# Kernel tuning notes

Measured on AMD Instinct MI355X. Metric: run time of the kernel, lower is better.

## Reference

```python
import jax, jax.numpy as jnp
import numpy as np

N = 50000       # nodes
E = 800000      # edges (before self loops)
F_IN = 256      # num_features
HID = 64        # hidden_dim
HEADS = 4       # num_heads
NEG = 0.2       # negative_slope
LN_EPS = 1e-5


def setup_inputs() -> dict:
    key = jax.random.key(0)
    ks = jax.random.split(key, 24)
    g = lambda k, shape, s=0.05: jax.random.normal(k, shape, jnp.float32) * s
    inp = {
        "x": jax.random.normal(ks[0], (N, F_IN), jnp.float32),
        "edge_index": jax.random.randint(ks[1], (2, E), 0, N, jnp.int32),
        # gat1: in=F_IN, out=HID per head, HEADS heads, concat=True
        "W1": g(ks[2], (HEADS * HID, F_IN)),
        "att_src1": g(ks[3], (HEADS, HID)),
        "att_dst1": g(ks[4], (HEADS, HID)),
        "b1": g(ks[5], (HEADS * HID,)),
        # gat2: in=HEADS*HID, out=HID, 1 head
        "W2": g(ks[6], (HID, HEADS * HID)),
        "att_src2": g(ks[7], (1, HID)),
        "att_dst2": g(ks[8], (1, HID)),
        "b2": g(ks[9], (HID,)),
        # lin_in residual projection
        "lin_w": g(ks[10], (HID, F_IN)),
        "lin_b": g(ks[11], (HID,)),
        # LayerNorm
        "gamma": jnp.ones((HID,), jnp.float32),
        "beta": jnp.zeros((HID,), jnp.float32),
        # GRU (1 layer, input=HID, hidden=HID), gate order r,z,n as in torch
        "w_ih": g(ks[12], (3 * HID, HID)),
        "w_hh": g(ks[13], (3 * HID, HID)),
        "b_ih": g(ks[14], (3 * HID,)),
        "b_hh": g(ks[15], (3 * HID,)),
        # fc head -> 3 classes
        "fc_w": g(ks[16], (3, HID)),
        "fc_b": g(ks[17], (3,)),
    }
    return inp


def gat_conv(x, W, att_src, att_dst, bias, src, dst, heads, n_nodes):
    """PyG-style GATConv (eval mode: no dropout). src/dst include self loops."""
    h = (x @ W.T).reshape(n_nodes, heads, -1)            # [N,H,C]
    a_src = jnp.einsum('nhc,hc->nh', h, att_src)          # [N,H]
    a_dst = jnp.einsum('nhc,hc->nh', h, att_dst)
    e = jax.nn.leaky_relu(a_src[src] + a_dst[dst], NEG)   # [E',H]
    m = jax.ops.segment_max(e, dst, num_segments=n_nodes) # scatter-softmax over dst
    e = jnp.exp(e - m[dst])
    s = jax.ops.segment_sum(e, dst, num_segments=n_nodes)
    alpha = e / s[dst]                                    # [E',H]
    out = jax.ops.segment_sum(alpha[:, :, None] * h[src], dst, num_segments=n_nodes)
    return out.reshape(n_nodes, -1) + bias                # concat heads + bias


def reference(x, edge_index, W1, att_src1, att_dst1, b1, W2, att_src2, att_dst2, b2,
              lin_w, lin_b, gamma, beta, w_ih, w_hh, b_ih, b_hh, fc_w, fc_b):
    n = x.shape[0]
    loops = jnp.arange(n, dtype=edge_index.dtype)
    src = jnp.concatenate([edge_index[0], loops])  # add_self_loops=True default
    dst = jnp.concatenate([edge_index[1], loops])

    h = jax.nn.leaky_relu(gat_conv(x, W1, att_src1, att_dst1, b1, src, dst, HEADS, n), NEG)
    # F.dropout is identity in eval mode
    h = gat_conv(h, W2, att_src2, att_dst2, b2, src, dst, 1, n)
    h = jax.nn.leaky_relu(h, NEG)
    # LayerNorm (torch uses biased variance)
    mu = h.mean(-1, keepdims=True)
    var = ((h - mu) ** 2).mean(-1, keepdims=True)
    h = (h - mu) / jnp.sqrt(var + LN_EPS) * gamma + beta
    h = h + x @ lin_w.T + lin_b
    # single-step GRU with h0 = 0 (seq_len == 1)
    gi = h @ w_ih.T + b_ih                 # [N,3C]
    i_r, i_z, i_n = jnp.split(gi, 3, axis=-1)
    h_r, h_z, h_n = jnp.split(b_hh, 3)     # W_hh @ 0 == 0
    r = jax.nn.sigmoid(i_r + h_r)
    z = jax.nn.sigmoid(i_z + h_z)
    ng = jnp.tanh(i_n + r * h_n)
    hy = (1.0 - z) * ng                    # + z * h_prev(=0)
    return hy @ fc_w.T + fc_b              # [N,3]
```

## Files before the change

kernel.cpp:

```cpp
#include <hip/hip_runtime.h>
#include <hip/hip_bf16.h>

#define N_NODES 50000
#define N_EDGES 800000
#define F_IN 256
#define HID 64
#define HEADS 4
#define NEG 0.2f
#define LN_EPS 1e-5f

typedef _Float16 half8 __attribute__((ext_vector_type(8)));
typedef _Float16 half4v __attribute__((ext_vector_type(4)));
typedef _Float16 half2v __attribute__((ext_vector_type(2)));
typedef float floatx4 __attribute__((ext_vector_type(4)));

union H2U { unsigned u; half2v h; };
union H8U { half8 v; half2v h2[4]; };

__device__ __forceinline__ float wave_sum(float v) {
    #pragma unroll
    for (int o = 32; o > 0; o >>= 1) v += __shfl_xor(v, o, 64);
    return v;
}
__device__ __forceinline__ float leaky(float x) { return x > 0.0f ? x : NEG * x; }

__global__ void prep_kernel(const int* __restrict__ src, const int* __restrict__ dst,
                            int* __restrict__ deg, int* __restrict__ colb,
                            const float* __restrict__ W1, const float* __restrict__ lin_w,
                            const float* __restrict__ W2, const float* __restrict__ w_ih,
                            _Float16* __restrict__ B1big, _Float16* __restrict__ W2h,
                            _Float16* __restrict__ w_ihh,
                            int E, int Etot, int SB) {
    if ((int)blockIdx.x < SB) {
        int e = blockIdx.x * 256 + threadIdx.x;
        if (e >= Etot) return;
        int s, d;
        if (e < E) { s = src[e]; d = dst[e]; }
        else       { s = d = e - E; }
        int pos = atomicAdd(&deg[d], 1);
        if (pos < 64) colb[d * 64 + pos] = s;
        return;
    }
    int rel = ((blockIdx.x - SB) * 256 + threadIdx.x) * 4;
    const float* s; _Float16* d;
    if      (rel < 65536) { s = W1; d = B1big; }
    else if ((rel -= 65536) < 16384) { s = lin_w; d = B1big + 65536; }
    else if ((rel -= 16384) < 16384) { s = W2; d = W2h; }
    else if ((rel -= 16384) < 12288) { s = w_ih; d = w_ihh; }
    else return;
    float4 v = *(const float4*)(s + rel);
    half4v h;
    h[0] = (_Float16)v.x; h[1] = (_Float16)v.y;
    h[2] = (_Float16)v.z; h[3] = (_Float16)v.w;
    *(half4v*)(d + rel) = h;
}

__device__ __forceinline__ half8 load_a8(const _Float16* p) { return *(const half8*)p; }
__device__ __forceinline__ half8 load_a8(const float* p) {
    float4 f0 = *(const float4*)p;
    float4 f1 = *(const float4*)(p + 4);
    half8 h;
    h[0] = (_Float16)f0.x; h[1] = (_Float16)f0.y;
    h[2] = (_Float16)f0.z; h[3] = (_Float16)f0.w;
    h[4] = (_Float16)f1.x; h[5] = (_Float16)f1.y;
    h[6] = (_Float16)f1.z; h[7] = (_Float16)f1.w;
    return h;
}

template<int NT, int H, typename OutT, typename AT>
__global__ __launch_bounds__(256, 2)
void gemm_mfma(const AT* __restrict__ A, const _Float16* __restrict__ B,
               const float* __restrict__ bias, OutT* __restrict__ Cout,
               const float* __restrict__ att_s, const float* __restrict__ att_d,
               float* __restrict__ a_srcO, float* __restrict__ a_dstO,
               int M, int K, int bias_mode) {
    constexpr int Nc = NT * 16;
    constexpr int BROW = 40;
    constexpr int BTILE = Nc * BROW * 2;
    constexpr int TILEB = 16 * Nc * sizeof(OutT);
    constexpr int SM = (BTILE > 4 * TILEB) ? BTILE : 4 * TILEB;
    __shared__ __align__(16) char smem[SM];
    _Float16* sB = (_Float16*)smem;
    int tid = threadIdx.x;
    int w = tid >> 6, lane = tid & 63;
    int m_base = blockIdx.x * 64 + w * 16;
    bool active = (m_base < M);
    int r = lane & 15, q = lane >> 4;
    const AT* ap = A + (size_t)(m_base + r) * K + q * 8;
    floatx4 acc[NT];
    #pragma unroll
    for (int t = 0; t < NT; ++t) acc[t] = (floatx4){0.f, 0.f, 0.f, 0.f};
    half8 a_next = {};
    if (active) a_next = load_a8(ap);
    for (int k0 = 0; k0 < K; k0 += 32) {
        for (int i = tid; i < Nc * 4; i += 256) {
            int row = i >> 2, seg = i & 3;
            *(half8*)(sB + row * BROW + seg * 8) =
                *(const half8*)(B + (size_t)row * K + k0 + seg * 8);
        }
        __syncthreads();
        half8 a = a_next;
        if (active && k0 + 32 < K) a_next = load_a8(ap + k0 + 32);
        if (active) {
            half8 b[NT];
            #pragma unroll
            for (int t = 0; t < NT; ++t)
                b[t] = *(const half8*)(sB + (t * 16 + r) * BROW + q * 8);
            #pragma unroll
            for (int t = 0; t < NT; ++t)
                acc[t] = __builtin_amdgcn_mfma_f32_16x16x32_f16(a, b[t], acc[t], 0, 0, 0);
        }
        __syncthreads();
    }
    if (active) {
        OutT* st = (OutT*)(smem + w * TILEB);
        #pragma unroll
        for (int t = 0; t < NT; ++t) {
            int cc = t * 16 + r;
            float bv = 0.f;
            if (bias_mode == 1) bv = bias[cc];
            else if (bias_mode == 2 && cc >= 256) bv = bias[cc - 256];
            #pragma unroll
            for (int rr = 0; rr < 4; ++rr)
                st[(q * 4 + rr) * Nc + cc] = (OutT)(acc[t][rr] + bv);
        }
        constexpr int NISS = TILEB / 1024;
        const int4* src = (const int4*)st;
        int4* dst = (int4*)((char*)Cout + (size_t)m_base * (Nc * sizeof(OutT)));
        #pragma unroll
        for (int i = 0; i < NISS; ++i) dst[i * 64 + lane] = src[i * 64 + lane];
        if constexpr (H > 0) {
            float ps[H][4], pd[H][4];
            #pragma unroll
            for (int h = 0; h < H; ++h) {
                #pragma unroll
                for (int rr = 0; rr < 4; ++rr) { ps[h][rr] = 0.f; pd[h][rr] = 0.f; }
                #pragma unroll
                for (int tt = 0; tt < 4; ++tt) {
                    int t = h * 4 + tt;
                    float as = att_s[t * 16 + r];
                    float ad = att_d[t * 16 + r];
                    #pragma unroll
                    for (int rr = 0; rr < 4; ++rr) {
                        ps[h][rr] += acc[t][rr] * as;
                        pd[h][rr] += acc[t][rr] * ad;
                    }
                }
            }
            #pragma unroll
            for (int m = 1; m < 16; m <<= 1) {
                #pragma unroll
                for (int h = 0; h < H; ++h)
                    #pragma unroll
                    for (int rr = 0; rr < 4; ++rr) {
                        ps[h][rr] += __shfl_xor(ps[h][rr], m, 64);
                        pd[h][rr] += __shfl_xor(pd[h][rr], m, 64);
                    }
            }
            if (r == 0) {
                #pragma unroll
                for (int rr = 0; rr < 4; ++rr) {
                    int gm = m_base + q * 4 + rr;
                    #pragma unroll
                    for (int h = 0; h < H; ++h) {
                        a_srcO[gm * H + h] = ps[h][rr];
                        a_dstO[gm * H + h] = pd[h][rr];
                    }
                }
            }
        }
    }
}

__global__ void gat_agg4(const _Float16* __restrict__ h, const float* __restrict__ a_src,
                         const float* __restrict__ a_dst, const int* __restrict__ degA,
                         const int* __restrict__ colb, const float* __restrict__ bias,
                         _Float16* __restrict__ outp, int N) {
    int w = threadIdx.x >> 6, lane = threadIdx.x & 63;
    int i = blockIdx.x * 4 + w;
    if (i >= N) return;
    __shared__ unsigned alphS[4][256];
    __shared__ int      scolS[4][64];
    unsigned* alph = alphS[w];
    int*      scol = scolS[w];
    int deg = degA[i];
    deg = deg > 64 ? 64 : deg;
    float4 ad4 = *(const float4*)(a_dst + i * 4);

    float e0 = 0.f, e1 = 0.f, e2 = 0.f, e3 = 0.f; int s = 0;
    if (lane < deg) {
        s = colb[i * 64 + lane];
        float4 as4 = *(const float4*)(a_src + (size_t)s * 4);
        e0 = __expf(leaky(as4.x + ad4.x));
        e1 = __expf(leaky(as4.y + ad4.y));
        e2 = __expf(leaky(as4.z + ad4.z));
        e3 = __expf(leaky(as4.w + ad4.w));
    }
    float s0 = wave_sum(e0), s1 = wave_sum(e1), s2 = wave_sum(e2), s3 = wave_sum(e3);
    float4 al = make_float4(0.f, 0.f, 0.f, 0.f);
    int so = 0;
    if (lane < deg) {
        al = make_float4(e0 / s0, e1 / s1, e2 / s2, e3 / s3);
        so = s * 640;
    }
    H2U p0, p1, p2, p3;
    _Float16 t0 = (_Float16)al.x; p0.h = (half2v){t0, t0};
    _Float16 t1 = (_Float16)al.y; p1.h = (half2v){t1, t1};
    _Float16 t2 = (_Float16)al.z; p2.h = (half2v){t2, t2};
    _Float16 t3 = (_Float16)al.w; p3.h = (half2v){t3, t3};
    *(uint4*)(alph + lane * 4) = make_uint4(p0.u, p1.u, p2.u, p3.u);
    scol[lane] = so;
    int half32 = lane >> 5;
    int fl = lane & 31;
    int flb = fl * 16;
    int ahofs = half32 * 4 + (fl >> 3);
    const char* hB = (const char*)h;
    float acc[8];
    #pragma unroll
    for (int k = 0; k < 8; ++k) acc[k] = 0.f;
    int dpad = (deg + 7) & ~7;
    for (int j = 0; j < dpad; j += 8) {
        int o0 = scol[j + half32];
        int o1 = scol[j + 2 + half32];
        int o2 = scol[j + 4 + half32];
        int o3 = scol[j + 6 + half32];
        H8U v0, v1, v2, v3;
        v0.v = *(const half8*)(hB + (flb + o0));
        v1.v = *(const half8*)(hB + (flb + o1));
        v2.v = *(const half8*)(hB + (flb + o2));
        v3.v = *(const half8*)(hB + (flb + o3));
        H2U a0, a1, a2, a3;
        a0.u = alph[j * 4 + ahofs];
        a1.u = alph[j * 4 + 8 + ahofs];
        a2.u = alph[j * 4 + 16 + ahofs];
        a3.u = alph[j * 4 + 24 + ahofs];
        #pragma unroll
        for (int p = 0; p < 4; ++p) {
            half2v hp = a0.h * v0.h2[p];
            hp = __builtin_elementwise_fma(a1.h, v1.h2[p], hp);
            hp = __builtin_elementwise_fma(a2.h, v2.h2[p], hp);
            hp = __builtin_elementwise_fma(a3.h, v3.h2[p], hp);
            acc[p * 2]     += (float)hp[0];
            acc[p * 2 + 1] += (float)hp[1];
        }
    }
    #pragma unroll
    for (int k = 0; k < 8; ++k) acc[k] += __shfl_xor(acc[k], 32, 64);
    if (lane < 32) {
        half8 o8;
        #pragma unroll
        for (int k = 0; k < 8; ++k)
            o8[k] = (_Float16)leaky(acc[k] + bias[fl * 8 + k]);
        *(half8*)(outp + (size_t)i * 256 + fl * 8) = o8;
    }
}

__global__ void gat_agg1_ln(const _Float16* __restrict__ h, const float* __restrict__ a_src,
                            const float* __restrict__ a_dst, const int* __restrict__ degA,
                            const int* __restrict__ colb, const float* __restrict__ bias,
                            const _Float16* __restrict__ linh, const float* __restrict__ gamma,
                            const float* __restrict__ beta, _Float16* __restrict__ hresh,
                            int N) {
    int w = threadIdx.x >> 6, lane = threadIdx.x & 63;
    int i = blockIdx.x * 4 + w;
    if (i >= N) return;
    __shared__ unsigned alphS[4][80];
    __shared__ int      scolS[4][80];
    unsigned* alph = alphS[w];
    int*      scol = scolS[w];
    int deg = degA[i];
    deg = deg > 64 ? 64 : deg;
    float ad = a_dst[i];
    int f0 = (lane & 7) * 8;
    float acc[8];
    #pragma unroll
    for (int k = 0; k < 8; ++k) acc[k] = 0.f;

    float e = 0.f; int s = 0;
    if (lane < deg) {
        s = colb[i * 64 + lane];
        e = __expf(leaky(a_src[s] + ad));
    }
    float ss = wave_sum(e);
    H2U pa; pa.u = 0;
    int so = 0;
    if (lane < deg) {
        _Float16 ah = (_Float16)(e / ss);
        pa.h = (half2v){ah, ah};
        so = s << 7;
    }
    alph[lane] = pa.u;
    scol[lane] = so;
    if (lane < 16) { alph[64 + lane] = 0; scol[64 + lane] = 0; }
    int g = lane >> 3;
    int fb = (lane & 7) * 16;
    const char* hB = (const char*)h;
    int dpad = (deg + 15) & ~15;
    for (int j = 0; j < dpad; j += 16) {
        int o0 = scol[j + g];
        int o1 = scol[j + 8 + g];
        H8U v0, v1;
        v0.v = *(const half8*)(hB + (fb + o0));
        v1.v = *(const half8*)(hB + (fb + o1));
        H2U a0, a1;
        a0.u = alph[j + g];
        a1.u = alph[j + 8 + g];
        #pragma unroll
        for (int p = 0; p < 4; ++p) {
            half2v hp = a0.h * v0.h2[p];
            hp = __builtin_elementwise_fma(a1.h, v1.h2[p], hp);
            acc[p * 2]     += (float)hp[0];
            acc[p * 2 + 1] += (float)hp[1];
        }
    }
    #pragma unroll
    for (int k = 0; k < 8; ++k) {
        acc[k] += __shfl_xor(acc[k], 8, 64);
        acc[k] += __shfl_xor(acc[k], 16, 64);
        acc[k] += __shfl_xor(acc[k], 32, 64);
    }
    float4 b0 = *(const float4*)(bias + f0);
    float4 b1 = *(const float4*)(bias + f0 + 4);
    float o[8];
    o[0] = leaky(acc[0] + b0.x); o[1] = leaky(acc[1] + b0.y);
    o[2] = leaky(acc[2] + b0.z); o[3] = leaky(acc[3] + b0.w);
    o[4] = leaky(acc[4] + b1.x); o[5] = leaky(acc[5] + b1.y);
    o[6] = leaky(acc[6] + b1.z); o[7] = leaky(acc[7] + b1.w);
    float ls = 0.f;
    #pragma unroll
    for (int k = 0; k < 8; ++k) ls += o[k];
    ls += __shfl_xor(ls, 1, 64); ls += __shfl_xor(ls, 2, 64); ls += __shfl_xor(ls, 4, 64);
    float mu = ls * (1.0f / 64.0f);
    float lq = 0.f;
    #pragma unroll
    for (int k = 0; k < 8; ++k) { o[k] -= mu; lq += o[k] * o[k]; }
    lq += __shfl_xor(lq, 1, 64); lq += __shfl_xor(lq, 2, 64); lq += __shfl_xor(lq, 4, 64);
    float rstd = rsqrtf(lq * (1.0f / 64.0f) + LN_EPS);
    float4 g0 = *(const float4*)(gamma + f0);
    float4 g1 = *(const float4*)(gamma + f0 + 4);
    float4 be0 = *(const float4*)(beta + f0);
    float4 be1 = *(const float4*)(beta + f0 + 4);
    half8 l8 = *(const half8*)(linh + (size_t)i * 320 + f0);
    if (lane < 8) {
        half8 hv;
        hv[0] = (_Float16)(o[0] * rstd * g0.x + be0.x + (float)l8[0]);
        hv[1] = (_Float16)(o[1] * rstd * g0.y + be0.y + (float)l8[1]);
        hv[2] = (_Float16)(o[2] * rstd * g0.z + be0.z + (float)l8[2]);
        hv[3] = (_Float16)(o[3] * rstd * g0.w + be0.w + (float)l8[3]);
        hv[4] = (_Float16)(o[4] * rstd * g1.x + be1.x + (float)l8[4]);
        hv[5] = (_Float16)(o[5] * rstd * g1.y + be1.y + (float)l8[5]);
        hv[6] = (_Float16)(o[6] * rstd * g1.z + be1.z + (float)l8[6]);
        hv[7] = (_Float16)(o[7] * rstd * g1.w + be1.w + (float)l8[7]);
        *(half8*)(hresh + (size_t)i * 64 + f0) = hv;
    }
}

__global__ __launch_bounds__(256, 2)
void gemm_gru(const _Float16* __restrict__ A, const _Float16* __restrict__ B,
              const float* __restrict__ b_ih, const float* __restrict__ b_hh,
              const float* __restrict__ fc_w, const float* __restrict__ fc_b,
              float* __restrict__ outp, int M) {
    const int K = 64, NT = 12, Nc = 192;
    constexpr int BROW = 40;
    __shared__ __align__(16) char smem[4 * 16 * 192 * 2];
    _Float16* sB = (_Float16*)smem;
    int tid = threadIdx.x;
    int w = tid >> 6, lane = tid & 63;
    int m_base = blockIdx.x * 64 + w * 16;
    bool active = (m_base < M);
    int r = lane & 15, q = lane >> 4;
    const _Float16* ap = A + (size_t)(m_base + r) * K + q * 8;
    floatx4 acc[NT];
    #pragma unroll
    for (int t = 0; t < NT; ++t) acc[t] = (floatx4){0.f, 0.f, 0.f, 0.f};
    half8 a_next = {};
    if (active) a_next = *(const half8*)ap;
    for (int k0 = 0; k0 < K; k0 += 32) {
        for (int i = tid; i < Nc * 4; i += 256) {
            int row = i >> 2, seg = i & 3;
            *(half8*)(sB + row * BROW + seg * 8) =
                *(const half8*)(B + (size_t)row * K + k0 + seg * 8);
        }
        __syncthreads();
        half8 a = a_next;
        if (active && k0 + 32 < K) a_next = *(const half8*)(ap + k0 + 32);
        if (active) {
            half8 b[NT];
            #pragma unroll
            for (int t = 0; t < NT; ++t)
                b[t] = *(const half8*)(sB + (t * 16 + r) * BROW + q * 8);
            #pragma unroll
            for (int t = 0; t < NT; ++t)
                acc[t] = __builtin_amdgcn_mfma_f32_16x16x32_f16(a, b[t], acc[t], 0, 0, 0);
        }
        __syncthreads();
    }
    if (!active) return;
    _Float16* sw = (_Float16*)smem + w * 16 * 192;
    #pragma unroll
    for (int t = 0; t < NT; ++t) {
        int cc = t * 16 + r;
        float bv = b_ih[cc];
        #pragma unroll
        for (int rr = 0; rr < 4; ++rr)
            sw[(q * 4 + rr) * Nc + cc] = (_Float16)(acc[t][rr] + bv);
    }
    float br_[4], bz_[4], bn_[4], f0_[4], f1_[4], f2_[4];
    *(float4*)br_ = *(const float4*)(b_hh + r * 4);
    *(float4*)bz_ = *(const float4*)(b_hh + 64 + r * 4);
    *(float4*)bn_ = *(const float4*)(b_hh + 128 + r * 4);
    *(float4*)f0_ = *(const float4*)(fc_w + r * 4);
    *(float4*)f1_ = *(const float4*)(fc_w + 64 + r * 4);
    *(float4*)f2_ = *(const float4*)(fc_w + 128 + r * 4);
    #pragma unroll
    for (int rr = 0; rr < 4; ++rr) {
        int row = q * 4 + rr;
        const _Float16* g = sw + row * Nc;
        half4v ir4 = *(const half4v*)(g + r * 4);
        half4v iz4 = *(const half4v*)(g + 64 + r * 4);
        half4v in4 = *(const half4v*)(g + 128 + r * 4);
        float p0 = 0.f, p1 = 0.f, p2 = 0.f;
        #pragma unroll
        for (int k = 0; k < 4; ++k) {
            float rg = 1.0f / (1.0f + __expf(-((float)ir4[k] + br_[k])));
            float zg = 1.0f / (1.0f + __expf(-((float)iz4[k] + bz_[k])));
            float ng = tanhf((float)in4[k] + rg * bn_[k]);
            float hy = (1.0f - zg) * ng;
            p0 += hy * f0_[k]; p1 += hy * f1_[k]; p2 += hy * f2_[k];
        }
        #pragma unroll
        for (int o = 1; o <= 8; o <<= 1) {
            p0 += __shfl_xor(p0, o, 64);
            p1 += __shfl_xor(p1, o, 64);
            p2 += __shfl_xor(p2, o, 64);
        }
        if (r == 0) {
            int gm = m_base + row;
            outp[(size_t)gm * 3 + 0] = p0 + fc_b[0];
            outp[(size_t)gm * 3 + 1] = p1 + fc_b[1];
            outp[(size_t)gm * 3 + 2] = p2 + fc_b[2];
        }
    }
}

extern "C" void kernel_launch(void* const* d_in, const int* in_sizes, int n_in,
                              void* d_out, int out_size, void* d_ws, size_t ws_size,
                              hipStream_t stream) {
    const float* x        = (const float*)d_in[0];
    const int*   ei       = (const int*)d_in[1];
    const float* W1       = (const float*)d_in[2];
    const float* att_src1 = (const float*)d_in[3];
    const float* att_dst1 = (const float*)d_in[4];
    const float* b1       = (const float*)d_in[5];
    const float* W2       = (const float*)d_in[6];
    const float* att_src2 = (const float*)d_in[7];
    const float* att_dst2 = (const float*)d_in[8];
    const float* b2       = (const float*)d_in[9];
    const float* lin_w    = (const float*)d_in[10];
    const float* lin_b    = (const float*)d_in[11];
    const float* gamma    = (const float*)d_in[12];
    const float* beta     = (const float*)d_in[13];
    const float* w_ih     = (const float*)d_in[14];
    const float* b_ih     = (const float*)d_in[16];
    const float* b_hh     = (const float*)d_in[17];
    const float* fc_w     = (const float*)d_in[18];
    const float* fc_b     = (const float*)d_in[19];
    float* out = (float*)d_out;

    const int N = N_NODES, E = N_EDGES;
    const int Etot = E + N;
    char* ws = (char*)d_ws;

    size_t off = 0;
    auto alloc = [&](size_t bytes) {
        size_t o = off;
        off = (off + bytes + 255) & ~(size_t)255;
        return o;
    };
    int*      deg     = (int*)(ws + alloc((size_t)N * 4));
    int*      colb    = (int*)(ws + alloc((size_t)N * 64 * 4));
    float*    a_src1b = (float*)(ws + alloc((size_t)N * HEADS * 4));
    float*    a_dst1b = (float*)(ws + alloc((size_t)N * HEADS * 4));
    float*    a_src2b = (float*)(ws + alloc((size_t)N * 4));
    float*    a_dst2b = (float*)(ws + alloc((size_t)N * 4));
    _Float16* B1big   = (_Float16*)(ws + alloc((size_t)320 * 256 * 2));
    _Float16* W2h     = (_Float16*)(ws + alloc((size_t)64 * 256 * 2));
    _Float16* w_ihh   = (_Float16*)(ws + alloc((size_t)192 * 64 * 2));
    _Float16* h1L  = (_Float16*)(ws + alloc((size_t)32000000));
    char* r3 = ws + alloc((size_t)25600000);
    _Float16* o1h   = (_Float16*)r3;
    _Float16* hresh = (_Float16*)r3;
    char* r4 = ws + alloc((size_t)6400000);
    _Float16* h2h = (_Float16*)r4;

    hipMemsetAsync(deg, 0, (size_t)N * 4, stream);

    const int SB = (Etot + 255) / 256;
    const int CB = (110592 / 4 + 255) / 256;
    prep_kernel<<<SB + CB, 256, 0, stream>>>(ei, ei + E, deg, colb,
        W1, lin_w, W2, w_ih, B1big, W2h, w_ihh, E, Etot, SB);

    const int gmBlocks = (N + 63) / 64;
    const int aggBlocks = (N + 3) / 4;

    gemm_mfma<20, 4, _Float16, float><<<gmBlocks, 256, 0, stream>>>(x, B1big, lin_b, h1L,
        att_src1, att_dst1, a_src1b, a_dst1b, N, 256, 2);

    gat_agg4<<<aggBlocks, 256, 0, stream>>>(h1L, a_src1b, a_dst1b, deg, colb, b1, o1h, N);

    gemm_mfma<4, 1, _Float16, _Float16><<<gmBlocks, 256, 0, stream>>>(o1h, W2h, nullptr, h2h,
        att_src2, att_dst2, a_src2b, a_dst2b, N, 256, 0);

    gat_agg1_ln<<<aggBlocks, 256, 0, stream>>>(h2h, a_src2b, a_dst2b, deg, colb, b2,
        h1L + 256, gamma, beta, hresh, N);

    gemm_gru<<<gmBlocks, 256, 0, stream>>>(hresh, w_ihh, b_ih, b_hh, fc_w, fc_b, out, N);
}
```

Measured before the change: 323.7 us.

## Fuse edge bucketing and weight conversion into first GEMM launch

Merges the prep kernel (degree counting and adjacency bucketing, plus weight casts to fp16) into the first GAT projection GEMM as extra blocks of a single launch. The GEMM now converts W1/lin_w from fp32 to fp16 on the fly while staging them into shared memory, so the separate B1big conversion is dropped. This removes one launch and lets the atomic-heavy edge work overlap with the GEMM. The cost is that every GEMM block re-converts the fp32 weights and reads twice the weight bytes.

```diff
diff --git a/kernel.cpp b/kernel.cpp
--- a/kernel.cpp
+++ b/kernel.cpp
@@ -23,37 +23,6 @@
     return v;
 }
 __device__ __forceinline__ float leaky(float x) { return x > 0.0f ? x : NEG * x; }
-
-__global__ void prep_kernel(const int* __restrict__ src, const int* __restrict__ dst,
-                            int* __restrict__ deg, int* __restrict__ colb,
-                            const float* __restrict__ W1, const float* __restrict__ lin_w,
-                            const float* __restrict__ W2, const float* __restrict__ w_ih,
-                            _Float16* __restrict__ B1big, _Float16* __restrict__ W2h,
-                            _Float16* __restrict__ w_ihh,
-                            int E, int Etot, int SB) {
-    if ((int)blockIdx.x < SB) {
-        int e = blockIdx.x * 256 + threadIdx.x;
-        if (e >= Etot) return;
-        int s, d;
-        if (e < E) { s = src[e]; d = dst[e]; }
-        else       { s = d = e - E; }
-        int pos = atomicAdd(&deg[d], 1);
-        if (pos < 64) colb[d * 64 + pos] = s;
-        return;
-    }
-    int rel = ((blockIdx.x - SB) * 256 + threadIdx.x) * 4;
-    const float* s; _Float16* d;
-    if      (rel < 65536) { s = W1; d = B1big; }
-    else if ((rel -= 65536) < 16384) { s = lin_w; d = B1big + 65536; }
-    else if ((rel -= 16384) < 16384) { s = W2; d = W2h; }
-    else if ((rel -= 16384) < 12288) { s = w_ih; d = w_ihh; }
-    else return;
-    float4 v = *(const float4*)(s + rel);
-    half4v h;
-    h[0] = (_Float16)v.x; h[1] = (_Float16)v.y;
-    h[2] = (_Float16)v.z; h[3] = (_Float16)v.w;
-    *(half4v*)(d + rel) = h;
-}
 
 __device__ __forceinline__ half8 load_a8(const _Float16* p) { return *(const half8*)p; }
 __device__ __forceinline__ half8 load_a8(const float* p) {
@@ -65,6 +34,137 @@
     h[4] = (_Float16)f1.x; h[5] = (_Float16)f1.y;
     h[6] = (_Float16)f1.z; h[7] = (_Float16)f1.w;
     return h;
+}
+
+__global__ __launch_bounds__(256, 2)
+void front_kernel(const float* __restrict__ x,
+                  const float* __restrict__ W1, const float* __restrict__ lin_w,
+                  const float* __restrict__ lin_b,
+                  const float* __restrict__ att_s, const float* __restrict__ att_d,
+                  _Float16* __restrict__ h1L, float* __restrict__ a_srcO,
+                  float* __restrict__ a_dstO,
+                  const int* __restrict__ src, const int* __restrict__ dst,
+                  int* __restrict__ deg, int* __restrict__ colb,
+                  const float* __restrict__ W2, const float* __restrict__ w_ih,
+                  _Float16* __restrict__ W2h, _Float16* __restrict__ w_ihh,
+                  int M, int E, int Etot, int GB, int SB) {
+    if ((int)blockIdx.x >= GB) {
+        int b2 = blockIdx.x - GB;
+        if (b2 < SB) {
+            int e = b2 * 256 + threadIdx.x;
+            if (e >= Etot) return;
+            int s, d;
+            if (e < E) { s = src[e]; d = dst[e]; }
+            else       { s = d = e - E; }
+            int pos = atomicAdd(&deg[d], 1);
+            if (pos < 64) colb[d * 64 + pos] = s;
+        } else {
+            int rel = ((b2 - SB) * 256 + threadIdx.x) * 4;
+            const float* s; _Float16* dp;
+            if      (rel < 16384) { s = W2; dp = W2h; }
+            else if ((rel -= 16384) < 12288) { s = w_ih; dp = w_ihh; }
+            else return;
+            float4 v = *(const float4*)(s + rel);
+            half4v h;
+            h[0] = (_Float16)v.x; h[1] = (_Float16)v.y;
+            h[2] = (_Float16)v.z; h[3] = (_Float16)v.w;
+            *(half4v*)(dp + rel) = h;
+        }
+        return;
+    }
+    constexpr int NT = 20, Nc = 320, K = 256;
+    constexpr int BROW = 40;
+    constexpr int BTILE = Nc * BROW * 2;
+    constexpr int TILEB = 16 * Nc * 2;
+    constexpr int SM = (BTILE > 4 * TILEB) ? BTILE : 4 * TILEB;
+    __shared__ __align__(16) char smem[SM];
+    _Float16* sB = (_Float16*)smem;
+    int tid = threadIdx.x;
+    int w = tid >> 6, lane = tid & 63;
+    int m_base = blockIdx.x * 64 + w * 16;
+    bool active = (m_base < M);
+    int r = lane & 15, q = lane >> 4;
+    const float* ap = x + (size_t)(m_base + r) * K + q * 8;
+    floatx4 acc[NT];
+    #pragma unroll
+    for (int t = 0; t < NT; ++t) acc[t] = (floatx4){0.f, 0.f, 0.f, 0.f};
+    half8 a_next = {};
+    if (active) a_next = load_a8(ap);
+    for (int k0 = 0; k0 < K; k0 += 32) {
+        for (int i = tid; i < Nc * 4; i += 256) {
+            int row = i >> 2, seg = i & 3;
+            const float* bp = (row < 256 ? W1 + (size_t)row * 256
+                                         : lin_w + (size_t)(row - 256) * 256) + k0 + seg * 8;
+            *(half8*)(sB + row * BROW + seg * 8) = load_a8(bp);
+        }
+        __syncthreads();
+        half8 a = a_next;
+        if (active && k0 + 32 < K) a_next = load_a8(ap + k0 + 32);
+        if (active) {
+            half8 b[NT];
+            #pragma unroll
+            for (int t = 0; t < NT; ++t)
+                b[t] = *(const half8*)(sB + (t * 16 + r) * BROW + q * 8);
+            #pragma unroll
+            for (int t = 0; t < NT; ++t)
+                acc[t] = __builtin_amdgcn_mfma_f32_16x16x32_f16(a, b[t], acc[t], 0, 0, 0);
+        }
+        __syncthreads();
+    }
+    if (active) {
+        _Float16* st = (_Float16*)(smem + w * TILEB);
+        #pragma unroll
+        for (int t = 0; t < NT; ++t) {
+            int cc = t * 16 + r;
+            float bv = (cc >= 256) ? lin_b[cc - 256] : 0.f;
+            #pragma unroll
+            for (int rr = 0; rr < 4; ++rr)
+                st[(q * 4 + rr) * Nc + cc] = (_Float16)(acc[t][rr] + bv);
+        }
+        constexpr int NISS = TILEB / 1024;
+        const int4* srcp = (const int4*)st;
+        int4* dstp = (int4*)((char*)h1L + (size_t)m_base * (Nc * 2));
+        #pragma unroll
+        for (int i = 0; i < NISS; ++i) dstp[i * 64 + lane] = srcp[i * 64 + lane];
+        float ps[HEADS][4], pd[HEADS][4];
+        #pragma unroll
+        for (int h = 0; h < HEADS; ++h) {
+            #pragma unroll
+            for (int rr = 0; rr < 4; ++rr) { ps[h][rr] = 0.f; pd[h][rr] = 0.f; }
+            #pragma unroll
+            for (int tt = 0; tt < 4; ++tt) {
+                int t = h * 4 + tt;
+                float as = att_s[t * 16 + r];
+                float ad = att_d[t * 16 + r];
+                #pragma unroll
+                for (int rr = 0; rr < 4; ++rr) {
+                    ps[h][rr] += acc[t][rr] * as;
+                    pd[h][rr] += acc[t][rr] * ad;
+                }
+            }
+        }
+        #pragma unroll
+        for (int m = 1; m < 16; m <<= 1) {
+            #pragma unroll
+            for (int h = 0; h < HEADS; ++h)
+                #pragma unroll
+                for (int rr = 0; rr < 4; ++rr) {
+                    ps[h][rr] += __shfl_xor(ps[h][rr], m, 64);
+                    pd[h][rr] += __shfl_xor(pd[h][rr], m, 64);
+                }
+        }
+        if (r == 0) {
+            #pragma unroll
+            for (int rr = 0; rr < 4; ++rr) {
+                int gm = m_base + q * 4 + rr;
+                #pragma unroll
+                for (int h = 0; h < HEADS; ++h) {
+                    a_srcO[gm * HEADS + h] = ps[h][rr];
+                    a_dstO[gm * HEADS + h] = pd[h][rr];
+                }
+            }
+        }
+    }
 }
 
 template<int NT, int H, typename OutT, typename AT>
@@ -119,7 +219,6 @@
             int cc = t * 16 + r;
             float bv = 0.f;
             if (bias_mode == 1) bv = bias[cc];
-            else if (bias_mode == 2 && cc >= 256) bv = bias[cc - 256];
             #pragma unroll
             for (int rr = 0; rr < 4; ++rr)
                 st[(q * 4 + rr) * Nc + cc] = (OutT)(acc[t][rr] + bv);
@@ -483,7 +582,6 @@
     float*    a_dst1b = (float*)(ws + alloc((size_t)N * HEADS * 4));
     float*    a_src2b = (float*)(ws + alloc((size_t)N * 4));
     float*    a_dst2b = (float*)(ws + alloc((size_t)N * 4));
-    _Float16* B1big   = (_Float16*)(ws + alloc((size_t)320 * 256 * 2));
     _Float16* W2h     = (_Float16*)(ws + alloc((size_t)64 * 256 * 2));
     _Float16* w_ihh   = (_Float16*)(ws + alloc((size_t)192 * 64 * 2));
     _Float16* h1L  = (_Float16*)(ws + alloc((size_t)32000000));
@@ -495,16 +593,15 @@
 
     hipMemsetAsync(deg, 0, (size_t)N * 4, stream);
 
-    const int SB = (Etot + 255) / 256;
-    const int CB = (110592 / 4 + 255) / 256;
-    prep_kernel<<<SB + CB, 256, 0, stream>>>(ei, ei + E, deg, colb,
-        W1, lin_w, W2, w_ih, B1big, W2h, w_ihh, E, Etot, SB);
-
     const int gmBlocks = (N + 63) / 64;
     const int aggBlocks = (N + 3) / 4;
-
-    gemm_mfma<20, 4, _Float16, float><<<gmBlocks, 256, 0, stream>>>(x, B1big, lin_b, h1L,
-        att_src1, att_dst1, a_src1b, a_dst1b, N, 256, 2);
+    const int SB = (Etot + 255) / 256;
+    const int CB = ((16384 + 12288) / 4 + 255) / 256;
+
+    front_kernel<<<gmBlocks + SB + CB, 256, 0, stream>>>(x, W1, lin_w, lin_b,
+        att_src1, att_dst1, h1L, a_src1b, a_dst1b,
+        ei, ei + E, deg, colb, W2, w_ih, W2h, w_ihh,
+        N, E, Etot, gmBlocks, SB);
 
     gat_agg4<<<aggBlocks, 256, 0, stream>>>(h1L, a_src1b, a_dst1b, deg, colb, b1, o1h, N);
 
```

Measured after the change: 299.3 us (median of 3 runs). -7.5%, faster.
